# Optimization experiments

Measured on AMD Instinct MI355X. Metric: run time of the kernel, lower is better.

Reference implementation:

```python
import jax, jax.numpy as jnp
import numpy as np

EPS = 1e-6

def _normalize(x):
    # x / sqrt(max(||x||^2, eps)) -- matches torch clamp_min on squared norm
    n2 = jnp.sum(x * x, axis=-1, keepdims=True)
    return x / jnp.sqrt(jnp.maximum(n2, EPS))

def setup_inputs() -> dict:
    key = jax.random.key(0)
    k1, k2, k3, k4 = jax.random.split(key, 4)
    B, N, M, D = 2, 4096, 4096, 256
    state_dim, out_dim = 2 * D, 512
    em1 = jax.random.normal(k1, (B, N, D), dtype=jnp.float32)
    em2 = jax.random.normal(k2, (B, M, D), dtype=jnp.float32)
    # fc params (torch Linear init: U(-1/sqrt(in), 1/sqrt(in)))
    bound = 1.0 / np.sqrt(state_dim)
    W = jax.random.uniform(k3, (out_dim, state_dim), minval=-bound, maxval=bound, dtype=jnp.float32)
    b = jax.random.uniform(k4, (out_dim,), minval=-bound, maxval=bound, dtype=jnp.float32)
    return {"em1": em1, "em2": em2, "W": W, "b": b}

def reference(em1, em2, W, b):
    # cosine similarity = normalized GEMM (same math as broadcast mul+sum)
    s = jnp.einsum('bnd,bmd->bnm', _normalize(em1), _normalize(em2))  # [B,N,M]
    soft = jax.nn.softmax(s, axis=-1)
    x = jnp.einsum('bnm,bmd->bnd', soft, em2)                          # [B,N,D]
    emb = jnp.concatenate([em1, x], axis=-1)                           # [B,N,2D]
    h = jax.nn.relu(emb @ W.T + b)                                     # [B,N,out_dim]
    return h
```

## Files before the change

kernel.cpp:

```cpp
#include <hip/hip_runtime.h>

#define BATCH 2
#define NQ    4096
#define MK    4096
#define DD    256
#define ODIM  512
#define SDIM  512
#define NROWS (BATCH * NQ)
#define BM    64
#define BK    64
#define MSPLIT 4
#define MCHUNK (MK / MSPLIT)
#define NKT    (MCHUNK / BK)
#define XSPLIT (BATCH * NQ * DD)

#define NCH_E1 (NROWS * DD / 8)
#define NCH_K  NCH_E1
#define NCH_V  NCH_E1
#define NCH_W  (ODIM * SDIM / 8)
#define RN_BLOCKS 4096

typedef short bf16x8 __attribute__((ext_vector_type(8)));
typedef float f32x16 __attribute__((ext_vector_type(16)));

__device__ __forceinline__ float bf2f(unsigned short h) {
    unsigned int u = ((unsigned int)h) << 16;
    float f;
    __builtin_memcpy(&f, &u, 4);
    return f;
}
__device__ __forceinline__ unsigned short f2bf(float f) {
    unsigned int u;
    __builtin_memcpy(&u, &f, 4);
    u = (u + 0x7FFFu + ((u >> 16) & 1u)) >> 16;
    return (unsigned short)u;
}
union frag_cast { uint4 u; bf16x8 b; unsigned short h[8]; };
__device__ __forceinline__ bf16x8 ldg_frag(const unsigned short* p) {
    frag_cast c;
    c.u = *(const uint4*)p;
    return c.b;
}
__device__ __forceinline__ void load_lds16(const unsigned short* g, unsigned short* l) {
    __builtin_amdgcn_global_load_lds(
        (const __attribute__((address_space(1))) void*)g,
        (__attribute__((address_space(3))) void*)l, 16, 0, 0);
}

__global__ void prep_kernel(const float* em1, const float* em2, const float* W,
                            float* rn, unsigned short* e1sw, unsigned short* ksw,
                            unsigned short* vsw, unsigned short* wsw) {
    int bid = blockIdx.x;
    if (bid < RN_BLOCKS) {
        int row  = bid * 4 + (threadIdx.x >> 6);
        int lane = threadIdx.x & 63;
        const float* src = (row < NROWS) ? em1 + (size_t)row * DD
                                         : em2 + (size_t)(row - NROWS) * DD;
        float4 v = *(const float4*)(src + lane * 4);
        float ss = v.x * v.x + v.y * v.y + v.z * v.z + v.w * v.w;
#pragma unroll
        for (int off = 1; off < 64; off <<= 1) ss += __shfl_xor(ss, off, 64);
        if (lane == 0) rn[row] = rsqrtf(fmaxf(ss, 1e-6f));
        return;
    }
    int cg = (bid - RN_BLOCKS) * 256 + threadIdx.x;
    if (cg < NCH_E1 + NCH_K) {
        const float* src;
        unsigned short* dst;
        int c0;
        if (cg < NCH_E1) { src = em1; dst = e1sw; c0 = cg; }
        else             { src = em2; dst = ksw;  c0 = cg - NCH_E1; }
        int g = c0 >> 10, c = c0 & 1023;
        int r31 = c & 31;
        int k0  = (c >> 5) * 8;
        const float* sp = src + (size_t)(g * 32 + r31) * DD + k0;
        float4 a = *(const float4*)sp;
        float4 b = *(const float4*)(sp + 4);
        ushort4 o1, o2;
        o1.x = f2bf(a.x); o1.y = f2bf(a.y); o1.z = f2bf(a.z); o1.w = f2bf(a.w);
        o2.x = f2bf(b.x); o2.y = f2bf(b.y); o2.z = f2bf(b.z); o2.w = f2bf(b.w);
        *(ushort4*)(dst + (size_t)c0 * 8)     = o1;
        *(ushort4*)(dst + (size_t)c0 * 8 + 4) = o2;
    } else if (cg < NCH_E1 + NCH_K + NCH_V) {
        int c0 = cg - (NCH_E1 + NCH_K);
        int b   = c0 >> 17;
        int r   = c0 & 131071;
        int dg  = r >> 14;
        int rr  = r & 16383;
        int oct = rr >> 5;
        int d31 = rr & 31;
        const float* sp = em2 + (size_t)(b * MK + oct * 8) * DD + dg * 32 + d31;
        ushort4 o1, o2;
        o1.x = f2bf(sp[0 * DD]); o1.y = f2bf(sp[1 * DD]);
        o1.z = f2bf(sp[2 * DD]); o1.w = f2bf(sp[3 * DD]);
        o2.x = f2bf(sp[4 * DD]); o2.y = f2bf(sp[5 * DD]);
        o2.z = f2bf(sp[6 * DD]); o2.w = f2bf(sp[7 * DD]);
        *(ushort4*)(vsw + (size_t)c0 * 8)     = o1;
        *(ushort4*)(vsw + (size_t)c0 * 8 + 4) = o2;
    } else {
        int c0 = cg - (NCH_E1 + NCH_K + NCH_V);
        if (c0 >= NCH_W) return;
        int g = c0 >> 11, c = c0 & 2047;
        int c31 = c & 31;
        int k0  = (c >> 5) * 8;
        const float* sp = W + (size_t)(g * 32 + c31) * SDIM + k0;
        float4 a = *(const float4*)sp;
        float4 b = *(const float4*)(sp + 4);
        ushort4 o1, o2;
        o1.x = f2bf(a.x); o1.y = f2bf(a.y); o1.z = f2bf(a.z); o1.w = f2bf(a.w);
        o2.x = f2bf(b.x); o2.y = f2bf(b.y); o2.z = f2bf(b.z); o2.w = f2bf(b.w);
        *(ushort4*)(wsw + (size_t)c0 * 8)     = o1;
        *(ushort4*)(wsw + (size_t)c0 * 8 + 4) = o2;
    }
}

__global__ __launch_bounds__(256, 2)
void flash_kernel(const unsigned short* e1sw, const unsigned short* ksw,
                  const unsigned short* vsw, const float* rn,
                  unsigned short* Xp, float* lbuf) {
    __shared__ unsigned short Ks[16384];
    __shared__ unsigned short Vs[16384];
    __shared__ unsigned short Ps[BM * 72];
    __shared__ float ls[2][BM];
    int tid = threadIdx.x, lane = tid & 63, w = tid >> 6;
    int l31 = lane & 31, lhalf = lane >> 5;
    int wr = w & 1, wc = w >> 1;
    int bid    = blockIdx.x;
    int mchunk = bid >> 7;
    int rowblk = bid & 127;
    int batch  = rowblk >> 6;
    int r0     = rowblk * BM;

    const unsigned short* qbase =
        e1sw + (size_t)(rowblk * 2 + wr) * 8192 + lhalf * 256 + l31 * 8;
    bf16x8 qf[16];
#pragma unroll
    for (int s = 0; s < 16; s++) qf[s] = ldg_frag(qbase + s * 512);

    float rqv[16];
#pragma unroll
    for (int i = 0; i < 16; i++) {
        int m = (i & 3) + 8 * (i >> 2) + 4 * lhalf;
        rqv[i] = rn[r0 + wr * 32 + m];
    }
    const float* rnk = rn + NROWS + batch * MK + mchunk * MCHUNK;

    const unsigned short* kchunk = ksw + (size_t)(batch * 128 + mchunk * 32) * 8192;
    const unsigned short* vbase  = vsw + (size_t)batch * 1048576 +
                                   (size_t)(mchunk * 128) * 256;

    f32x16 xacc[4];
#pragma unroll
    for (int t = 0; t < 4; t++)
#pragma unroll
        for (int i = 0; i < 16; i++) xacc[t][i] = 0.f;
    float lpart[16];
#pragma unroll
    for (int i = 0; i < 16; i++) lpart[i] = 0.f;

    for (int kt = 0; kt < NKT; kt++) {
        __syncthreads();
        {
            const unsigned short* ksrc = kchunk + (size_t)kt * 16384;
#pragma unroll
            for (int it = 0; it < 8; it++)
                load_lds16(ksrc + it * 2048 + tid * 8, &Ks[it * 2048 + tid * 8]);
            const unsigned short* vsrc = vbase + (size_t)(kt * 8) * 256;
#pragma unroll
            for (int dg = 0; dg < 8; dg++)
                load_lds16(vsrc + (size_t)dg * 131072 + tid * 8, &Vs[dg * 2048 + tid * 8]);
        }
        __syncthreads();
        f32x16 sA, sB;
#pragma unroll
        for (int i = 0; i < 16; i++) { sA[i] = 0.f; sB[i] = 0.f; }
        const unsigned short* kb = &Ks[wc * 8192 + lhalf * 256 + l31 * 8];
#pragma unroll
        for (int s = 0; s < 16; s += 2) {
            bf16x8 b0 = ldg_frag(kb + s * 512);
            bf16x8 b1 = ldg_frag(kb + (s + 1) * 512);
            sA = __builtin_amdgcn_mfma_f32_32x32x16_bf16(qf[s],     b0, sA, 0, 0, 0);
            sB = __builtin_amdgcn_mfma_f32_32x32x16_bf16(qf[s + 1], b1, sB, 0, 0, 0);
        }
        float rk = rnk[kt * BK + wc * 32 + l31];
#pragma unroll
        for (int i = 0; i < 16; i++) {
            float p = __expf((sA[i] + sB[i]) * rqv[i] * rk - 1.0f);
            unsigned short pb = f2bf(p);
            lpart[i] += bf2f(pb);
            int m = wr * 32 + (i & 3) + 8 * (i >> 2) + 4 * lhalf;
            Ps[m * 72 + wc * 32 + l31] = pb;
        }
        __syncthreads();
#pragma unroll
        for (int ks = 0; ks < 4; ks++) {
            frag_cast ac;
            ac.u = *(const uint4*)&Ps[(wr * 32 + l31) * 72 + ks * 16 + lhalf * 8];
#pragma unroll
            for (int nt = 0; nt < 4; nt++) {
                bf16x8 bf = ldg_frag(&Vs[((wc * 4 + nt) * 8 + ks * 2 + lhalf) * 256 + l31 * 8]);
                xacc[nt] = __builtin_amdgcn_mfma_f32_32x32x16_bf16(ac.b, bf, xacc[nt], 0, 0, 0);
            }
        }
    }

#pragma unroll
    for (int i = 0; i < 16; i++) {
        float v = lpart[i];
#pragma unroll
        for (int off = 1; off < 32; off <<= 1) v += __shfl_xor(v, off, 64);
        if (l31 == 0) {
            int m = wr * 32 + (i & 3) + 8 * (i >> 2) + 4 * lhalf;
            ls[wc][m] = v;
        }
    }
    __syncthreads();
    if (tid < BM)
        lbuf[(size_t)mchunk * NROWS + r0 + tid] = ls[0][tid] + ls[1][tid];

    unsigned short* xout = Xp + (size_t)mchunk * XSPLIT +
                           (size_t)(rowblk * 2 + wr) * 8192;
#pragma unroll
    for (int nt = 0; nt < 4; nt++) {
        int dcol = wc * 128 + nt * 32 + l31;
        int cbase = (dcol >> 3) * 256 + (dcol & 7);
#pragma unroll
        for (int i = 0; i < 16; i++) {
            int m = (i & 3) + 8 * (i >> 2) + 4 * lhalf;
            xout[cbase + m * 8] = f2bf(xacc[nt][i]);
        }
    }
}

__global__ void reduce_kernel(const unsigned short* Xp, const float* lbuf,
                              unsigned short* xnsw) {
    int cg  = blockIdx.x * 256 + threadIdx.x;
    int row = (cg >> 10) * 32 + (cg & 31);
    float l = lbuf[row] + lbuf[NROWS + row] +
              lbuf[2 * NROWS + row] + lbuf[3 * NROWS + row];
    float rinv = 1.0f / l;
    const unsigned short* p = Xp + (size_t)cg * 8;
    frag_cast p0, p1, p2, p3, u;
    p0.u = *(const uint4*)p;
    p1.u = *(const uint4*)(p + (size_t)XSPLIT);
    p2.u = *(const uint4*)(p + 2 * (size_t)XSPLIT);
    p3.u = *(const uint4*)(p + 3 * (size_t)XSPLIT);
#pragma unroll
    for (int j = 0; j < 8; j++) {
        float f = bf2f(p0.h[j]) + bf2f(p1.h[j]) + bf2f(p2.h[j]) + bf2f(p3.h[j]);
        u.h[j] = f2bf(f * rinv);
    }
    *(uint4*)(xnsw + (size_t)cg * 8) = u.u;
}

__global__ __launch_bounds__(256, 4)
void final_gemm(const unsigned short* e1sw, const unsigned short* xnsw,
                const unsigned short* wsw, const float* bias, float* out) {
    int tid = threadIdx.x, lane = tid & 63, w = tid >> 6;
    int l31 = lane & 31, lhalf = lane >> 5;
    int wr = w & 1, wc = w >> 1;
    int bid = blockIdx.x;
    int rb = bid & 127, cb = bid >> 7;
    int gA = rb * 2 + wr;
    int gB = cb * 2 + wc;

    f32x16 acc;
#pragma unroll
    for (int i = 0; i < 16; i++) acc[i] = 0.f;

    const unsigned short* abase = e1sw + (size_t)gA * 8192 + lhalf * 256 + l31 * 8;
    const unsigned short* xbase = xnsw + (size_t)gA * 8192 + lhalf * 256 + l31 * 8;
    const unsigned short* bbase = wsw  + (size_t)gB * 16384 + lhalf * 256 + l31 * 8;

    for (int kk = 0; kk < 32; kk++) {
        bf16x8 afr = (kk < 16) ? ldg_frag(abase + kk * 512)
                               : ldg_frag(xbase + (kk - 16) * 512);
        bf16x8 bfr = ldg_frag(bbase + kk * 512);
        acc = __builtin_amdgcn_mfma_f32_32x32x16_bf16(afr, bfr, acc, 0, 0, 0);
    }

    int col = gB * 32 + l31;
    float bb = bias[col];
#pragma unroll
    for (int i = 0; i < 16; i++) {
        int row = gA * 32 + (i & 3) + 8 * (i >> 2) + 4 * lhalf;
        float v = acc[i] + bb;
        v = v > 0.f ? v : 0.f;
        out[(size_t)row * ODIM + col] = v;
    }
}

extern "C" void kernel_launch(void* const* d_in, const int* in_sizes, int n_in,
                              void* d_out, int out_size, void* d_ws, size_t ws_size,
                              hipStream_t stream) {
    const float* em1  = (const float*)d_in[0];
    const float* em2  = (const float*)d_in[1];
    const float* W    = (const float*)d_in[2];
    const float* bias = (const float*)d_in[3];
    float* out = (float*)d_out;

    char* ws = (char*)d_ws;
    unsigned short* e1sw = (unsigned short*)ws;
    unsigned short* ksw  = e1sw + (size_t)NROWS * DD;
    unsigned short* vsw  = ksw  + (size_t)NROWS * DD;
    unsigned short* wsw  = vsw  + (size_t)BATCH * DD * MK;
    unsigned short* Xp   = wsw  + (size_t)ODIM * SDIM;
    unsigned short* xnsw = Xp   + 4 * (size_t)XSPLIT;
    float* lbuf = (float*)(xnsw + (size_t)NROWS * DD);
    float* rn   = lbuf + 4 * (size_t)NROWS;

    const int swz_blocks = (NCH_E1 + NCH_K + NCH_V + NCH_W + 255) / 256;
    prep_kernel<<<RN_BLOCKS + swz_blocks, 256, 0, stream>>>(
        em1, em2, W, rn, e1sw, ksw, vsw, wsw);
    flash_kernel<<<(NROWS / BM) * MSPLIT, 256, 0, stream>>>(e1sw, ksw, vsw, rn, Xp, lbuf);
    reduce_kernel<<<NCH_E1 / 256, 256, 0, stream>>>(Xp, lbuf, xnsw);
    final_gemm<<<(NROWS / 64) * (ODIM / 64), 256, 0, stream>>>(
        e1sw, xnsw, wsw, bias, out);
}
```

Before: 142.2 us.

## Fuse row-norm into bf16 swizzle, prescale K, fold reduce into final GEMM

The prep kernel now does the row-norm pass and the bf16 swizzle of em1/em2 in the same pass, so those inputs are read once instead of twice. K rows are prescaled by their inverse norm, which removes the per-key norm load and multiply in the flash inner loop. The separate reduce kernel is folded into final_gemm: each block combines the four split-M partials for 32 rows into LDS and then computes all 512 output columns. The price is fewer, heavier final-GEMM blocks that each stream the whole W from global memory, plus an extra bf16 rounding of the normalized K.

```diff
diff --git a/kernel.cpp b/kernel.cpp
--- a/kernel.cpp
+++ b/kernel.cpp
@@ -14,10 +14,8 @@
 #define NKT    (MCHUNK / BK)
 #define XSPLIT (BATCH * NQ * DD)
 
-#define NCH_E1 (NROWS * DD / 8)
-#define NCH_K  NCH_E1
-#define NCH_V  NCH_E1
-#define NCH_W  (ODIM * SDIM / 8)
+#define NCH_V (NROWS * DD / 8)
+#define NCH_W (ODIM * SDIM / 8)
 #define RN_BLOCKS 4096
 
 typedef short bf16x8 __attribute__((ext_vector_type(8)));
@@ -51,40 +49,33 @@
                             float* rn, unsigned short* e1sw, unsigned short* ksw,
                             unsigned short* vsw, unsigned short* wsw) {
     int bid = blockIdx.x;
+    int tid = threadIdx.x;
     if (bid < RN_BLOCKS) {
-        int row  = bid * 4 + (threadIdx.x >> 6);
-        int lane = threadIdx.x & 63;
-        const float* src = (row < NROWS) ? em1 + (size_t)row * DD
-                                         : em2 + (size_t)(row - NROWS) * DD;
+        int row  = bid * 4 + (tid >> 6);
+        int lane = tid & 63;
+        bool is_q = row < NROWS;
+        int r = is_q ? row : row - NROWS;
+        const float* src = (is_q ? em1 : em2) + (size_t)r * DD;
         float4 v = *(const float4*)(src + lane * 4);
         float ss = v.x * v.x + v.y * v.y + v.z * v.z + v.w * v.w;
 #pragma unroll
         for (int off = 1; off < 64; off <<= 1) ss += __shfl_xor(ss, off, 64);
-        if (lane == 0) rn[row] = rsqrtf(fmaxf(ss, 1e-6f));
+        float rs = rsqrtf(fmaxf(ss, 1e-6f));
+        float scale = is_q ? 1.0f : rs;
+        if (is_q && lane == 0) rn[r] = rs;
+        unsigned short* dst = is_q ? e1sw : ksw;
+        int g = r >> 5, r31 = r & 31;
+        int k = lane * 4;
+        ushort4 o;
+        o.x = f2bf(v.x * scale); o.y = f2bf(v.y * scale);
+        o.z = f2bf(v.z * scale); o.w = f2bf(v.w * scale);
+        *(ushort4*)(dst + ((size_t)g * 1024 + (k >> 3) * 32 + r31) * 8 + (k & 7)) = o;
         return;
     }
-    int cg = (bid - RN_BLOCKS) * 256 + threadIdx.x;
-    if (cg < NCH_E1 + NCH_K) {
-        const float* src;
-        unsigned short* dst;
-        int c0;
-        if (cg < NCH_E1) { src = em1; dst = e1sw; c0 = cg; }
-        else             { src = em2; dst = ksw;  c0 = cg - NCH_E1; }
-        int g = c0 >> 10, c = c0 & 1023;
-        int r31 = c & 31;
-        int k0  = (c >> 5) * 8;
-        const float* sp = src + (size_t)(g * 32 + r31) * DD + k0;
-        float4 a = *(const float4*)sp;
-        float4 b = *(const float4*)(sp + 4);
-        ushort4 o1, o2;
-        o1.x = f2bf(a.x); o1.y = f2bf(a.y); o1.z = f2bf(a.z); o1.w = f2bf(a.w);
-        o2.x = f2bf(b.x); o2.y = f2bf(b.y); o2.z = f2bf(b.z); o2.w = f2bf(b.w);
-        *(ushort4*)(dst + (size_t)c0 * 8)     = o1;
-        *(ushort4*)(dst + (size_t)c0 * 8 + 4) = o2;
-    } else if (cg < NCH_E1 + NCH_K + NCH_V) {
-        int c0 = cg - (NCH_E1 + NCH_K);
-        int b   = c0 >> 17;
-        int r   = c0 & 131071;
+    int cg = (bid - RN_BLOCKS) * 256 + tid;
+    if (cg < NCH_V) {
+        int b   = cg >> 17;
+        int r   = cg & 131071;
         int dg  = r >> 14;
         int rr  = r & 16383;
         int oct = rr >> 5;
@@ -95,10 +86,10 @@
         o1.z = f2bf(sp[2 * DD]); o1.w = f2bf(sp[3 * DD]);
         o2.x = f2bf(sp[4 * DD]); o2.y = f2bf(sp[5 * DD]);
         o2.z = f2bf(sp[6 * DD]); o2.w = f2bf(sp[7 * DD]);
-        *(ushort4*)(vsw + (size_t)c0 * 8)     = o1;
-        *(ushort4*)(vsw + (size_t)c0 * 8 + 4) = o2;
+        *(ushort4*)(vsw + (size_t)cg * 8)     = o1;
+        *(ushort4*)(vsw + (size_t)cg * 8 + 4) = o2;
     } else {
-        int c0 = cg - (NCH_E1 + NCH_K + NCH_V);
+        int c0 = cg - NCH_V;
         if (c0 >= NCH_W) return;
         int g = c0 >> 11, c = c0 & 2047;
         int c31 = c & 31;
@@ -143,7 +134,6 @@
         int m = (i & 3) + 8 * (i >> 2) + 4 * lhalf;
         rqv[i] = rn[r0 + wr * 32 + m];
     }
-    const float* rnk = rn + NROWS + batch * MK + mchunk * MCHUNK;
 
     const unsigned short* kchunk = ksw + (size_t)(batch * 128 + mchunk * 32) * 8192;
     const unsigned short* vbase  = vsw + (size_t)batch * 1048576 +
@@ -182,10 +172,9 @@
             sA = __builtin_amdgcn_mfma_f32_32x32x16_bf16(qf[s],     b0, sA, 0, 0, 0);
             sB = __builtin_amdgcn_mfma_f32_32x32x16_bf16(qf[s + 1], b1, sB, 0, 0, 0);
         }
-        float rk = rnk[kt * BK + wc * 32 + l31];
 #pragma unroll
         for (int i = 0; i < 16; i++) {
-            float p = __expf((sA[i] + sB[i]) * rqv[i] * rk - 1.0f);
+            float p = __expf((sA[i] + sB[i]) * rqv[i] - 1.0f);
             unsigned short pb = f2bf(p);
             lpart[i] += bf2f(pb);
             int m = wr * 32 + (i & 3) + 8 * (i >> 2) + 4 * lhalf;
@@ -232,61 +221,75 @@
     }
 }
 
-__global__ void reduce_kernel(const unsigned short* Xp, const float* lbuf,
-                              unsigned short* xnsw) {
-    int cg  = blockIdx.x * 256 + threadIdx.x;
-    int row = (cg >> 10) * 32 + (cg & 31);
-    float l = lbuf[row] + lbuf[NROWS + row] +
-              lbuf[2 * NROWS + row] + lbuf[3 * NROWS + row];
-    float rinv = 1.0f / l;
-    const unsigned short* p = Xp + (size_t)cg * 8;
-    frag_cast p0, p1, p2, p3, u;
-    p0.u = *(const uint4*)p;
-    p1.u = *(const uint4*)(p + (size_t)XSPLIT);
-    p2.u = *(const uint4*)(p + 2 * (size_t)XSPLIT);
-    p3.u = *(const uint4*)(p + 3 * (size_t)XSPLIT);
-#pragma unroll
-    for (int j = 0; j < 8; j++) {
-        float f = bf2f(p0.h[j]) + bf2f(p1.h[j]) + bf2f(p2.h[j]) + bf2f(p3.h[j]);
-        u.h[j] = f2bf(f * rinv);
-    }
-    *(uint4*)(xnsw + (size_t)cg * 8) = u.u;
-}
-
-__global__ __launch_bounds__(256, 4)
-void final_gemm(const unsigned short* e1sw, const unsigned short* xnsw,
-                const unsigned short* wsw, const float* bias, float* out) {
+__global__ __launch_bounds__(256, 2)
+void final_gemm(const unsigned short* e1sw, const unsigned short* Xp,
+                const float* lbuf, const unsigned short* wsw, const float* bias,
+                float* out) {
+    __shared__ unsigned short xn[8192];
+    __shared__ float lrinv[32];
     int tid = threadIdx.x, lane = tid & 63, w = tid >> 6;
     int l31 = lane & 31, lhalf = lane >> 5;
-    int wr = w & 1, wc = w >> 1;
-    int bid = blockIdx.x;
-    int rb = bid & 127, cb = bid >> 7;
-    int gA = rb * 2 + wr;
-    int gB = cb * 2 + wc;
-
-    f32x16 acc;
-#pragma unroll
-    for (int i = 0; i < 16; i++) acc[i] = 0.f;
-
-    const unsigned short* abase = e1sw + (size_t)gA * 8192 + lhalf * 256 + l31 * 8;
-    const unsigned short* xbase = xnsw + (size_t)gA * 8192 + lhalf * 256 + l31 * 8;
-    const unsigned short* bbase = wsw  + (size_t)gB * 16384 + lhalf * 256 + l31 * 8;
+    int rg = blockIdx.x;
+
+    if (tid < 32) {
+        int row = rg * 32 + tid;
+        float l = lbuf[row] + lbuf[NROWS + row] +
+                  lbuf[2 * NROWS + row] + lbuf[3 * NROWS + row];
+        lrinv[tid] = 1.0f / l;
+    }
+    __syncthreads();
+
+    const unsigned short* xb = Xp + (size_t)rg * 8192;
+#pragma unroll
+    for (int it = 0; it < 4; it++) {
+        int c = it * 256 + tid;
+        const unsigned short* p = xb + c * 8;
+        frag_cast p0, p1, p2, p3, u;
+        p0.u = *(const uint4*)p;
+        p1.u = *(const uint4*)(p + (size_t)XSPLIT);
+        p2.u = *(const uint4*)(p + 2 * (size_t)XSPLIT);
+        p3.u = *(const uint4*)(p + 3 * (size_t)XSPLIT);
+        float rinv = lrinv[c & 31];
+#pragma unroll
+        for (int j = 0; j < 8; j++) {
+            float f = bf2f(p0.h[j]) + bf2f(p1.h[j]) + bf2f(p2.h[j]) + bf2f(p3.h[j]);
+            u.h[j] = f2bf(f * rinv);
+        }
+        *(uint4*)&xn[c * 8] = u.u;
+    }
+    __syncthreads();
+
+    f32x16 acc[4];
+#pragma unroll
+    for (int t = 0; t < 4; t++)
+#pragma unroll
+        for (int i = 0; i < 16; i++) acc[t][i] = 0.f;
+
+    const unsigned short* abase = e1sw + (size_t)rg * 8192 + lhalf * 256 + l31 * 8;
+    const unsigned short* bbase = wsw + lhalf * 256 + l31 * 8;
 
     for (int kk = 0; kk < 32; kk++) {
-        bf16x8 afr = (kk < 16) ? ldg_frag(abase + kk * 512)
-                               : ldg_frag(xbase + (kk - 16) * 512);
-        bf16x8 bfr = ldg_frag(bbase + kk * 512);
-        acc = __builtin_amdgcn_mfma_f32_32x32x16_bf16(afr, bfr, acc, 0, 0, 0);
-    }
-
-    int col = gB * 32 + l31;
-    float bb = bias[col];
-#pragma unroll
-    for (int i = 0; i < 16; i++) {
-        int row = gA * 32 + (i & 3) + 8 * (i >> 2) + 4 * lhalf;
-        float v = acc[i] + bb;
-        v = v > 0.f ? v : 0.f;
-        out[(size_t)row * ODIM + col] = v;
+        bf16x8 afr = (kk < 16)
+            ? ldg_frag(abase + kk * 512)
+            : ldg_frag(&xn[(kk - 16) * 512 + lhalf * 256 + l31 * 8]);
+#pragma unroll
+        for (int nt = 0; nt < 4; nt++) {
+            bf16x8 bfr = ldg_frag(bbase + (size_t)(w * 4 + nt) * 16384 + kk * 512);
+            acc[nt] = __builtin_amdgcn_mfma_f32_32x32x16_bf16(afr, bfr, acc[nt], 0, 0, 0);
+        }
+    }
+
+#pragma unroll
+    for (int nt = 0; nt < 4; nt++) {
+        int col = w * 128 + nt * 32 + l31;
+        float bb = bias[col];
+#pragma unroll
+        for (int i = 0; i < 16; i++) {
+            int row = rg * 32 + (i & 3) + 8 * (i >> 2) + 4 * lhalf;
+            float v = acc[nt][i] + bb;
+            v = v > 0.f ? v : 0.f;
+            out[(size_t)row * ODIM + col] = v;
+        }
     }
 }
 
@@ -305,15 +308,12 @@
     unsigned short* vsw  = ksw  + (size_t)NROWS * DD;
     unsigned short* wsw  = vsw  + (size_t)BATCH * DD * MK;
     unsigned short* Xp   = wsw  + (size_t)ODIM * SDIM;
-    unsigned short* xnsw = Xp   + 4 * (size_t)XSPLIT;
-    float* lbuf = (float*)(xnsw + (size_t)NROWS * DD);
+    float* lbuf = (float*)(Xp + 4 * (size_t)XSPLIT);
     float* rn   = lbuf + 4 * (size_t)NROWS;
 
-    const int swz_blocks = (NCH_E1 + NCH_K + NCH_V + NCH_W + 255) / 256;
-    prep_kernel<<<RN_BLOCKS + swz_blocks, 256, 0, stream>>>(
+    const int chunk_blocks = (NCH_V + NCH_W + 255) / 256;
+    prep_kernel<<<RN_BLOCKS + chunk_blocks, 256, 0, stream>>>(
         em1, em2, W, rn, e1sw, ksw, vsw, wsw);
     flash_kernel<<<(NROWS / BM) * MSPLIT, 256, 0, stream>>>(e1sw, ksw, vsw, rn, Xp, lbuf);
-    reduce_kernel<<<NCH_E1 / 256, 256, 0, stream>>>(Xp, lbuf, xnsw);
-    final_gemm<<<(NROWS / 64) * (ODIM / 64), 256, 0, stream>>>(
-        e1sw, xnsw, wsw, bias, out);
-}
+    final_gemm<<<NROWS / 32, 256, 0, stream>>>(e1sw, Xp, lbuf, wsw, bias, out);
+}
```

Result: slower. 145.5 us (+2.3%).

## Fuse norm and bf16 swizzle in prep; pre-scale keys by inverse norm

Applied to the files above, without the earlier changes.

The row-norm blocks now also convert each em1/em2 row to bf16 and write it in the swizzled layout, so the separate swizzle pass that reread em1 and em2 is gone. Key rows are pre-multiplied by their inverse norm before rounding, which removes the per-tile rk load and multiply from the flash inner loop. Query rows stay unscaled because e1sw is also used in the final GEMM. Keys are now rounded to bf16 after normalisation rather than before, which changes rounding slightly.

```diff
diff --git a/kernel.cpp b/kernel.cpp
--- a/kernel.cpp
+++ b/kernel.cpp
@@ -14,10 +14,8 @@
 #define NKT    (MCHUNK / BK)
 #define XSPLIT (BATCH * NQ * DD)
 
-#define NCH_E1 (NROWS * DD / 8)
-#define NCH_K  NCH_E1
-#define NCH_V  NCH_E1
-#define NCH_W  (ODIM * SDIM / 8)
+#define NCH_V (NROWS * DD / 8)
+#define NCH_W (ODIM * SDIM / 8)
 #define RN_BLOCKS 4096
 
 typedef short bf16x8 __attribute__((ext_vector_type(8)));
@@ -51,40 +49,33 @@
                             float* rn, unsigned short* e1sw, unsigned short* ksw,
                             unsigned short* vsw, unsigned short* wsw) {
     int bid = blockIdx.x;
+    int tid = threadIdx.x;
     if (bid < RN_BLOCKS) {
-        int row  = bid * 4 + (threadIdx.x >> 6);
-        int lane = threadIdx.x & 63;
-        const float* src = (row < NROWS) ? em1 + (size_t)row * DD
-                                         : em2 + (size_t)(row - NROWS) * DD;
+        int row  = bid * 4 + (tid >> 6);
+        int lane = tid & 63;
+        bool is_q = row < NROWS;
+        int r = is_q ? row : row - NROWS;
+        const float* src = (is_q ? em1 : em2) + (size_t)r * DD;
         float4 v = *(const float4*)(src + lane * 4);
         float ss = v.x * v.x + v.y * v.y + v.z * v.z + v.w * v.w;
 #pragma unroll
         for (int off = 1; off < 64; off <<= 1) ss += __shfl_xor(ss, off, 64);
-        if (lane == 0) rn[row] = rsqrtf(fmaxf(ss, 1e-6f));
+        float rs = rsqrtf(fmaxf(ss, 1e-6f));
+        float scale = is_q ? 1.0f : rs;
+        if (is_q && lane == 0) rn[r] = rs;
+        unsigned short* dst = is_q ? e1sw : ksw;
+        int g = r >> 5, r31 = r & 31;
+        int k = lane * 4;
+        ushort4 o;
+        o.x = f2bf(v.x * scale); o.y = f2bf(v.y * scale);
+        o.z = f2bf(v.z * scale); o.w = f2bf(v.w * scale);
+        *(ushort4*)(dst + ((size_t)g * 1024 + (k >> 3) * 32 + r31) * 8 + (k & 7)) = o;
         return;
     }
-    int cg = (bid - RN_BLOCKS) * 256 + threadIdx.x;
-    if (cg < NCH_E1 + NCH_K) {
-        const float* src;
-        unsigned short* dst;
-        int c0;
-        if (cg < NCH_E1) { src = em1; dst = e1sw; c0 = cg; }
-        else             { src = em2; dst = ksw;  c0 = cg - NCH_E1; }
-        int g = c0 >> 10, c = c0 & 1023;
-        int r31 = c & 31;
-        int k0  = (c >> 5) * 8;
-        const float* sp = src + (size_t)(g * 32 + r31) * DD + k0;
-        float4 a = *(const float4*)sp;
-        float4 b = *(const float4*)(sp + 4);
-        ushort4 o1, o2;
-        o1.x = f2bf(a.x); o1.y = f2bf(a.y); o1.z = f2bf(a.z); o1.w = f2bf(a.w);
-        o2.x = f2bf(b.x); o2.y = f2bf(b.y); o2.z = f2bf(b.z); o2.w = f2bf(b.w);
-        *(ushort4*)(dst + (size_t)c0 * 8)     = o1;
-        *(ushort4*)(dst + (size_t)c0 * 8 + 4) = o2;
-    } else if (cg < NCH_E1 + NCH_K + NCH_V) {
-        int c0 = cg - (NCH_E1 + NCH_K);
-        int b   = c0 >> 17;
-        int r   = c0 & 131071;
+    int cg = (bid - RN_BLOCKS) * 256 + tid;
+    if (cg < NCH_V) {
+        int b   = cg >> 17;
+        int r   = cg & 131071;
         int dg  = r >> 14;
         int rr  = r & 16383;
         int oct = rr >> 5;
@@ -95,10 +86,10 @@
         o1.z = f2bf(sp[2 * DD]); o1.w = f2bf(sp[3 * DD]);
         o2.x = f2bf(sp[4 * DD]); o2.y = f2bf(sp[5 * DD]);
         o2.z = f2bf(sp[6 * DD]); o2.w = f2bf(sp[7 * DD]);
-        *(ushort4*)(vsw + (size_t)c0 * 8)     = o1;
-        *(ushort4*)(vsw + (size_t)c0 * 8 + 4) = o2;
+        *(ushort4*)(vsw + (size_t)cg * 8)     = o1;
+        *(ushort4*)(vsw + (size_t)cg * 8 + 4) = o2;
     } else {
-        int c0 = cg - (NCH_E1 + NCH_K + NCH_V);
+        int c0 = cg - NCH_V;
         if (c0 >= NCH_W) return;
         int g = c0 >> 11, c = c0 & 2047;
         int c31 = c & 31;
@@ -143,7 +134,6 @@
         int m = (i & 3) + 8 * (i >> 2) + 4 * lhalf;
         rqv[i] = rn[r0 + wr * 32 + m];
     }
-    const float* rnk = rn + NROWS + batch * MK + mchunk * MCHUNK;
 
     const unsigned short* kchunk = ksw + (size_t)(batch * 128 + mchunk * 32) * 8192;
     const unsigned short* vbase  = vsw + (size_t)batch * 1048576 +
@@ -182,10 +172,9 @@
             sA = __builtin_amdgcn_mfma_f32_32x32x16_bf16(qf[s],     b0, sA, 0, 0, 0);
             sB = __builtin_amdgcn_mfma_f32_32x32x16_bf16(qf[s + 1], b1, sB, 0, 0, 0);
         }
-        float rk = rnk[kt * BK + wc * 32 + l31];
 #pragma unroll
         for (int i = 0; i < 16; i++) {
-            float p = __expf((sA[i] + sB[i]) * rqv[i] * rk - 1.0f);
+            float p = __expf((sA[i] + sB[i]) * rqv[i] - 1.0f);
             unsigned short pb = f2bf(p);
             lpart[i] += bf2f(pb);
             int m = wr * 32 + (i & 3) + 8 * (i >> 2) + 4 * lhalf;
@@ -309,11 +298,11 @@
     float* lbuf = (float*)(xnsw + (size_t)NROWS * DD);
     float* rn   = lbuf + 4 * (size_t)NROWS;
 
-    const int swz_blocks = (NCH_E1 + NCH_K + NCH_V + NCH_W + 255) / 256;
-    prep_kernel<<<RN_BLOCKS + swz_blocks, 256, 0, stream>>>(
+    const int chunk_blocks = (NCH_V + NCH_W + 255) / 256;
+    prep_kernel<<<RN_BLOCKS + chunk_blocks, 256, 0, stream>>>(
         em1, em2, W, rn, e1sw, ksw, vsw, wsw);
     flash_kernel<<<(NROWS / BM) * MSPLIT, 256, 0, stream>>>(e1sw, ksw, vsw, rn, Xp, lbuf);
-    reduce_kernel<<<NCH_E1 / 256, 256, 0, stream>>>(Xp, lbuf, xnsw);
+    reduce_kernel<<<NCH_V / 256, 256, 0, stream>>>(Xp, lbuf, xnsw);
     final_gemm<<<(NROWS / 64) * (ODIM / 64), 256, 0, stream>>>(
         e1sw, xnsw, wsw, bias, out);
 }
```

Result: faster. 137.1 us, median of 2 (-3.6%).
